# Performance work log

Hardware: AMD Instinct MI355X
Metric: run time of the kernel (lower is better)

The kernel has to match this reference:

```python
import jax, jax.numpy as jnp
import numpy as np
from jax import lax

B, T, D = 2, 2048, 2048
H = 8
DK = D // H          # head_qk_dim = 256 (expand_k forced to 1.0)
DV = D // H          # head_v_dim = 256 (expand_v forced to 1.0)
CONV_K = 4
CHUNK = 64
EPS = 1e-5
INTER = 2816         # int(2048*2*2/3)=2730 -> round up to multiple of 256


def setup_inputs() -> dict:
    key = jax.random.key(0)
    ks = jax.random.split(key, 14)
    s = 0.02
    return {
        "hidden_states": jax.random.normal(ks[0], (B, T, D), jnp.float32),
        "attn_norm_w": jnp.ones((D,), jnp.float32),
        "Wq": jax.random.normal(ks[1], (D, D), jnp.float32) * s,
        "Wk": jax.random.normal(ks[2], (D, D), jnp.float32) * s,
        "Wv": jax.random.normal(ks[3], (D, D), jnp.float32) * s,
        "Wg": jax.random.normal(ks[4], (D, D), jnp.float32) * s,
        "Wo": jax.random.normal(ks[5], (D, D), jnp.float32) * s,
        "conv_wq": jax.random.normal(ks[6], (D, CONV_K), jnp.float32) * 0.3,
        "conv_wk": jax.random.normal(ks[7], (D, CONV_K), jnp.float32) * 0.3,
        "conv_wv": jax.random.normal(ks[8], (D, CONV_K), jnp.float32) * 0.3,
        "gnorm_w": jnp.ones((DV,), jnp.float32),
        "mlp_norm_w": jnp.ones((D,), jnp.float32),
        "W_gate": jax.random.normal(ks[9], (D, 2 * INTER), jnp.float32) * s,
        "W_down": jax.random.normal(ks[10], (INTER, D), jnp.float32) * s,
    }


def rmsnorm(x, w, eps=EPS):
    return x * lax.rsqrt(jnp.mean(x * x, axis=-1, keepdims=True) + eps) * w


def short_conv_silu(x, w):
    # depthwise causal conv1d, kernel CONV_K, no bias, then SiLU. x: [B,T,C], w: [C,K]
    K = w.shape[-1]
    xp = jnp.pad(x, ((0, 0), (K - 1, 0), (0, 0)))
    y = sum(xp[:, i:i + x.shape[1], :] * w[None, None, :, i] for i in range(K))
    return jax.nn.silu(y)


def rope(x, cos, sin):
    # non-interleaved (GPT-NeoX style) rotary over full head dim. x: [B,T,H,d]
    x1, x2 = jnp.split(x, 2, axis=-1)
    c = cos[None, :, None, :]
    s = sin[None, :, None, :]
    return jnp.concatenate([x1 * c - x2 * s, x2 * c + x1 * s], axis=-1)


def chunk_retention(q, k, v, gamma, C=CHUNK):
    # q,k,v: [B,T,H,d]; gamma: [H]. o_t = q_t @ S_t, S_t = gamma*S_{t-1} + k_t^T v_t
    b, t, h, dk = q.shape
    dv = v.shape[-1]
    q = q * (dk ** -0.5)
    n = t // C
    to_chunks = lambda x: x.reshape(b, n, C, h, -1).transpose(1, 0, 3, 2, 4)  # [n,B,H,C,d]
    qc, kc, vc = map(to_chunks, (q, k, v))
    i = jnp.arange(C)
    diff = i[:, None] - i[None, :]
    pe = jnp.where(diff >= 0, diff, 0).astype(q.dtype)
    Dm = jnp.where(diff >= 0, gamma[:, None, None] ** pe, 0.0)       # [H,C,C] intra-chunk decay
    di = gamma[:, None] ** (i + 1).astype(q.dtype)                    # [H,C] decay from prev state
    dkc = gamma[:, None] ** (C - 1 - i).astype(q.dtype)               # [H,C] decay to chunk end
    gC = gamma ** C                                                   # [H]

    def step(S, xs):
        qi, ki, vi = xs                                              # [B,H,C,d]
        A = jnp.einsum('bhid,bhjd->bhij', qi, ki) * Dm
        o = A @ vi + jnp.einsum('bhid,bhde->bhie', qi, S) * di[None, :, :, None]
        S = S * gC[None, :, None, None] + jnp.einsum('bhjd,bhje->bhde', ki * dkc[None, :, :, None], vi)
        return S, o

    S0 = jnp.zeros((b, h, dk, dv), q.dtype)
    _, oc = lax.scan(step, S0, (qc, kc, vc))                          # [n,B,H,C,dv]
    return oc.transpose(1, 0, 3, 2, 4).reshape(b, t, h, dv)


def reference(hidden_states, attn_norm_w, Wq, Wk, Wv, Wg, Wo,
              conv_wq, conv_wk, conv_wv, gnorm_w, mlp_norm_w, W_gate, W_down):
    b, t, d = hidden_states.shape
    # --- MultiScaleRetention block (pre-norm) ---
    x = rmsnorm(hidden_states, attn_norm_w)
    q = short_conv_silu(x @ Wq, conv_wq)
    k = short_conv_silu(x @ Wk, conv_wk)
    v = short_conv_silu(x @ Wv, conv_wv)
    q = q.reshape(b, t, H, DK)
    k = k.reshape(b, t, H, DK)
    v = v.reshape(b, t, H, DV)
    # rotary embedding (base 10000), seqlen_offset=0
    inv_freq = 1.0 / (10000.0 ** (jnp.arange(0, DK, 2, dtype=jnp.float32) / DK))
    freqs = jnp.arange(t, dtype=jnp.float32)[:, None] * inv_freq[None, :]   # [T,DK/2]
    cos, sin = jnp.cos(freqs), jnp.sin(freqs)
    q, k = rope(q, cos, sin), rope(k, cos, sin)
    # per-head retention decay: gamma_h = 1 - 2^(-5-h)
    gamma = 1.0 - jnp.exp2(-5.0 - jnp.arange(H, dtype=jnp.float32))
    o = chunk_retention(q, k, v, gamma)                                     # [B,T,H,DV]
    # fused RMSNorm + swish gate
    g = (x @ Wg).reshape(b, t, H, DV)
    o = rmsnorm(o, gnorm_w) * (g * jax.nn.sigmoid(g))
    o = o.reshape(b, t, d) @ Wo
    h = hidden_states + o
    # --- gated MLP block (pre-norm, SwiGLU) ---
    y = rmsnorm(h, mlp_norm_w)
    gy = y @ W_gate
    gate, yv = jnp.split(gy, 2, axis=-1)
    y = (gate * jax.nn.sigmoid(gate) * yv) @ W_down
    return h + y
```

## Files before the change

### kernel.cpp

```cpp
#include <hip/hip_runtime.h>
#include <hip/hip_bf16.h>
#include <cstdint>
#include <cstddef>
#include <type_traits>


typedef __hip_bfloat16 bf16;
typedef __bf16 bf16x8 __attribute__((ext_vector_type(8)));
typedef __bf16 bf16x4 __attribute__((ext_vector_type(4)));
typedef float f32x4 __attribute__((ext_vector_type(4)));

#define DEVI __device__ __forceinline__

DEVI float bf2f(bf16 x) { return __bfloat162float(x); }
DEVI bf16 f2bf(float x) { return __float2bfloat16(x); }
DEVI float siluf(float x) { return x / (1.f + __expf(-x)); }
DEVI float log2gamma(int h) {
  return log1pf(-exp2f(-5.f - (float)h)) * 1.4426950408889634f;
}

#define GLL16(gp, lp)                                                  \
  __builtin_amdgcn_global_load_lds(                                    \
      (__attribute__((address_space(1))) void*)(gp),                   \
      (__attribute__((address_space(3))) void*)(lp), 16, 0, 0)

DEVI float blockSum256(float v) {
  #pragma unroll
  for (int off = 32; off; off >>= 1) v += __shfl_down(v, off, 64);
  __shared__ float sm[4];
  int lane = threadIdx.x & 63, w = threadIdx.x >> 6;
  if (lane == 0) sm[w] = v;
  __syncthreads();
  return sm[0] + sm[1] + sm[2] + sm[3];
}

__global__ void rmsnorm_k(const float* __restrict__ x, const float* __restrict__ w,
                          bf16* __restrict__ out) {
  long row = blockIdx.x;
  const float* xr = x + row * 2048;
  int i0 = threadIdx.x * 4;
  float4 v0 = *(const float4*)(xr + i0);
  float4 v1 = *(const float4*)(xr + 1024 + i0);
  float ss = v0.x*v0.x + v0.y*v0.y + v0.z*v0.z + v0.w*v0.w
           + v1.x*v1.x + v1.y*v1.y + v1.z*v1.z + v1.w*v1.w;
  ss = blockSum256(ss);
  float s = rsqrtf(ss * (1.f/2048.f) + 1e-5f);
  bf16* orow = out + row * 2048;
  orow[i0+0] = f2bf(v0.x*s*w[i0+0]); orow[i0+1] = f2bf(v0.y*s*w[i0+1]);
  orow[i0+2] = f2bf(v0.z*s*w[i0+2]); orow[i0+3] = f2bf(v0.w*s*w[i0+3]);
  orow[1024+i0+0] = f2bf(v1.x*s*w[1024+i0+0]); orow[1024+i0+1] = f2bf(v1.y*s*w[1024+i0+1]);
  orow[1024+i0+2] = f2bf(v1.z*s*w[1024+i0+2]); orow[1024+i0+3] = f2bf(v1.w*s*w[1024+i0+3]);
}

__global__ void rope_init(float2* __restrict__ tab) {
  int t = blockIdx.x, j = threadIdx.x;
  double inv = exp((double)(-j) * (9.210340371976184 / 128.0));
  double ang = fmod((double)t * inv, 6.283185307179586);
  tab[t * 128 + j] = make_float2((float)cos(ang), (float)sin(ang));
}

__global__ void transpose_w(const float* __restrict__ in, bf16* __restrict__ out,
                            int R, int C) {
  __shared__ float tile[32][33];
  int bx = blockIdx.x * 32, by = blockIdx.y * 32;
  int tx = threadIdx.x, ty = threadIdx.y;
  #pragma unroll
  for (int i = 0; i < 32; i += 8)
    tile[ty + i][tx] = in[(long)(by + ty + i) * C + bx + tx];
  __syncthreads();
  #pragma unroll
  for (int i = 0; i < 32; i += 8)
    out[(long)(bx + ty + i) * R + by + tx] = f2bf(tile[tx][ty + i]);
}

__global__ void transpose_w4(const float* __restrict__ w0, const float* __restrict__ w1,
                             const float* __restrict__ w2, const float* __restrict__ w3,
                             bf16* __restrict__ out) {
  __shared__ float tile[32][33];
  const float* in = blockIdx.z == 0 ? w0 : blockIdx.z == 1 ? w1
                   : blockIdx.z == 2 ? w2 : w3;
  int bx = blockIdx.x * 32, by = blockIdx.y * 32;
  int tx = threadIdx.x, ty = threadIdx.y;
  #pragma unroll
  for (int i = 0; i < 32; i += 8)
    tile[ty + i][tx] = in[(long)(by + ty + i) * 2048 + bx + tx];
  __syncthreads();
  long rbase = (long)blockIdx.z * 2048;
  #pragma unroll
  for (int i = 0; i < 32; i += 8)
    out[(rbase + bx + ty + i) * 2048 + by + tx] = f2bf(tile[tx][ty + i]);
}

__global__ void transpose_head(const bf16* __restrict__ in, bf16* __restrict__ out,
                               int withDecay) {
  __shared__ bf16 tile[32][33];
  const int bh = blockIdx.z, hh = bh & 7;
  const float lg = log2gamma(hh);
  const int t0 = blockIdx.y * 32, d0 = blockIdx.x * 32;
  const int tx = threadIdx.x, ty = threadIdx.y;
  const bf16* src = in + (long)bh * 2048 * 256;
  bf16* dst = out + (long)bh * 2048 * 256;
  #pragma unroll
  for (int i = 0; i < 32; i += 8) {
    int t = t0 + ty + i;
    float v = bf2f(src[(long)t * 256 + d0 + tx]);
    if (withDecay) v *= exp2f(lg * (float)(63 - (t & 63)));
    tile[ty + i][tx] = f2bf(v);
  }
  __syncthreads();
  #pragma unroll
  for (int i = 0; i < 32; i += 8)
    dst[(long)(d0 + ty + i) * 2048 + t0 + tx] = tile[tx][ty + i];
}

template <typename OUT_T, bool DO_ADD>
__global__ __launch_bounds__(256) void gemm_bt(
    const bf16* __restrict__ A, const bf16* __restrict__ Bt,
    OUT_T* __restrict__ C, int ldc, bf16* __restrict__ C2, int split,
    const float* __restrict__ addend, int M, int N, int K) {
  __shared__ alignas(16) bf16 As[128 * 32];
  __shared__ alignas(16) bf16 Bs[128 * 32];
  const int tid = threadIdx.x;
  const int lane = tid & 63, wid = tid >> 6;
  const int quad = lane >> 4, l16 = lane & 15;
  const int wm = wid >> 1, wn = wid & 1;
  const long bm = (long)blockIdx.x * 128;
  const long bn = (long)blockIdx.y * 128;

  const int srow = wid * 16 + (lane >> 2);
  const int scolP = (lane & 3) * 8;
  const int scolG = (((lane & 3) ^ ((srow >> 1) & 3))) * 8;
  const bf16* pa0 = A + (bm + srow) * (long)K + scolG;
  const bf16* pa1 = A + (bm + 64 + srow) * (long)K + scolG;
  const bf16* pb0 = Bt + (bn + srow) * (long)K + scolG;
  const bf16* pb1 = Bt + (bn + 64 + srow) * (long)K + scolG;
  bf16* la0 = As + srow * 32 + scolP;
  bf16* la1 = As + (64 + srow) * 32 + scolP;
  bf16* lb0 = Bs + srow * 32 + scolP;
  bf16* lb1 = Bs + (64 + srow) * 32 + scolP;

  const int fcol = ((quad ^ ((l16 >> 1) & 3)) * 8);

  const f32x4 zz = {0.f, 0.f, 0.f, 0.f};
  f32x4 acc[4][4];
  #pragma unroll
  for (int i = 0; i < 4; i++)
    #pragma unroll
    for (int j = 0; j < 4; j++) acc[i][j] = zz;

  for (int k0 = 0; k0 < K; k0 += 32) {
    GLL16(pa0 + k0, la0);
    GLL16(pa1 + k0, la1);
    GLL16(pb0 + k0, lb0);
    GLL16(pb1 + k0, lb1);
    __syncthreads();
    bf16x8 a[4], b[4];
    #pragma unroll
    for (int i = 0; i < 4; i++)
      a[i] = *(const bf16x8*)(As + (wm * 64 + i * 16 + l16) * 32 + fcol);
    #pragma unroll
    for (int j = 0; j < 4; j++)
      b[j] = *(const bf16x8*)(Bs + (wn * 64 + j * 16 + l16) * 32 + fcol);
    #pragma unroll
    for (int i = 0; i < 4; i++)
      #pragma unroll
      for (int j = 0; j < 4; j++)
        acc[i][j] = __builtin_amdgcn_mfma_f32_16x16x32_bf16(a[i], b[j], acc[i][j], 0, 0, 0);
    __syncthreads();
  }

  const bool sec = (bn >= split);
  #pragma unroll
  for (int i = 0; i < 4; i++)
    #pragma unroll
    for (int j = 0; j < 4; j++)
      #pragma unroll
      for (int r = 0; r < 4; r++) {
        long row = bm + wm * 64 + i * 16 + quad * 4 + r;
        long col = bn + wn * 64 + j * 16 + l16;
        float v = acc[i][j][r];
        if (sec) {
          C2[row * 2048 + (col - split)] = f2bf(v);
        } else {
          if constexpr (DO_ADD) v += addend[row * (long)ldc + col];
          if constexpr (std::is_same<OUT_T, float>::value)
            C[row * (long)ldc + col] = v;
          else
            C[row * (long)ldc + col] = f2bf(v);
        }
      }
}

__global__ void conv3(const bf16* __restrict__ u3,
                      const float* __restrict__ cwq, const float* __restrict__ cwk,
                      const float* __restrict__ cwv, const float2* __restrict__ rtab,
                      bf16* __restrict__ qb, bf16* __restrict__ kb,
                      bf16* __restrict__ vb) {
  const int bt = blockIdx.x;
  const int t = bt & 2047;
  const int b = bt >> 11;
  const int z = blockIdx.y;
  const int tid = threadIdx.x;
  const int h = tid >> 5;
  if (z < 2) {
    const float* cw = z == 0 ? cwq : cwk;
    bf16* out = z == 0 ? qb : kb;
    const float scale = z == 0 ? 0.0625f : 1.0f;
    const int j0 = (tid & 31) * 4;
    const int ch1 = h * 256 + j0, ch2 = ch1 + 128;
    const int c1 = z * 2048 + ch1, c2 = c1 + 128;
    f32x4 w1[4], w2[4];
    #pragma unroll
    for (int e = 0; e < 4; e++) {
      w1[e] = *(const f32x4*)(cw + (ch1 + e) * 4);
      w2[e] = *(const f32x4*)(cw + (ch2 + e) * 4);
    }
    float a1[4] = {0.f, 0.f, 0.f, 0.f}, a2[4] = {0.f, 0.f, 0.f, 0.f};
    #pragma unroll
    for (int i = 0; i < 4; i++) {
      int ts = t - 3 + i;
      if (ts >= 0) {
        const bf16* up = u3 + (long)(bt - 3 + i) * 6144;
        bf16x4 v1 = *(const bf16x4*)(up + c1);
        bf16x4 v2 = *(const bf16x4*)(up + c2);
        #pragma unroll
        for (int e = 0; e < 4; e++) {
          a1[e] += (float)v1[e] * w1[e][i];
          a2[e] += (float)v2[e] * w2[e][i];
        }
      }
    }
    f32x4 r01 = *(const f32x4*)(rtab + t * 128 + j0);
    f32x4 r23 = *(const f32x4*)(rtab + t * 128 + j0 + 2);
    float cs[4] = {r01[0], r01[2], r23[0], r23[2]};
    float sn[4] = {r01[1], r01[3], r23[1], r23[3]};
    bf16x4 o1, o2;
    #pragma unroll
    for (int e = 0; e < 4; e++) {
      float s1 = siluf(a1[e]), s2 = siluf(a2[e]);
      o1[e] = (__bf16)((s1 * cs[e] - s2 * sn[e]) * scale);
      o2[e] = (__bf16)((s2 * cs[e] + s1 * sn[e]) * scale);
    }
    long obase = ((long)(b * 8 + h) * 2048 + t) * 256;
    *(bf16x4*)(out + obase + j0) = o1;
    *(bf16x4*)(out + obase + 128 + j0) = o2;
  } else {
    const int e0 = (tid & 31) * 8;
    const int ch = h * 256 + e0;
    const int c = 4096 + ch;
    f32x4 w[8];
    #pragma unroll
    for (int e = 0; e < 8; e++) w[e] = *(const f32x4*)(cwv + (ch + e) * 4);
    float a[8] = {0.f, 0.f, 0.f, 0.f, 0.f, 0.f, 0.f, 0.f};
    #pragma unroll
    for (int i = 0; i < 4; i++) {
      int ts = t - 3 + i;
      if (ts >= 0) {
        bf16x8 v = *(const bf16x8*)(u3 + (long)(bt - 3 + i) * 6144 + c);
        #pragma unroll
        for (int e = 0; e < 8; e++) a[e] += (float)v[e] * w[e][i];
      }
    }
    bf16x8 o;
    #pragma unroll
    for (int e = 0; e < 8; e++) o[e] = (__bf16)siluf(a[e]);
    *(bf16x8*)(vb + ((long)(b * 8 + h) * 2048 + t) * 256 + e0) = o;
  }
}

__global__ __launch_bounds__(256) void chunk_outer(
    const bf16* __restrict__ vT, const bf16* __restrict__ kTd,
    bf16* __restrict__ states) {
  __shared__ alignas(16) bf16 lk[256 * 72];
  const int chunk = blockIdx.x, bh = blockIdx.y;
  const int tid = threadIdx.x;
  const int lane = tid & 63, wid = tid >> 6;
  const int quad = lane >> 4, l16 = lane & 15;
  const long base = (long)bh * 256 * 2048 + chunk * 64;

  #pragma unroll
  for (int it = 0; it < 8; it++) {
    int r = it * 32 + (tid >> 3);
    int cb = tid & 7;
    *(int4*)(lk + r * 72 + cb * 8) = *(const int4*)(kTd + base + (long)r * 2048 + cb * 8);
  }
  bf16x8 a[4][2];
  #pragma unroll
  for (int i = 0; i < 4; i++)
    #pragma unroll
    for (int ks = 0; ks < 2; ks++)
      a[i][ks] = *(const bf16x8*)(vT + base + (long)(wid * 64 + i * 16 + l16) * 2048 +
                                  ks * 32 + quad * 8);
  __syncthreads();

  bf16* sout = states + ((long)bh * 32 + chunk) * 65536;
  const f32x4 zz = {0.f, 0.f, 0.f, 0.f};
  for (int g = 0; g < 4; g++) {
    f32x4 acc[4][4];
    #pragma unroll
    for (int i = 0; i < 4; i++)
      #pragma unroll
      for (int j = 0; j < 4; j++) acc[i][j] = zz;
    #pragma unroll
    for (int ks = 0; ks < 2; ks++) {
      bf16x8 b[4];
      #pragma unroll
      for (int j = 0; j < 4; j++)
        b[j] = *(const bf16x8*)(lk + (g * 64 + j * 16 + l16) * 72 + ks * 32 + quad * 8);
      #pragma unroll
      for (int i = 0; i < 4; i++)
        #pragma unroll
        for (int j = 0; j < 4; j++)
          acc[i][j] = __builtin_amdgcn_mfma_f32_16x16x32_bf16(a[i][ks], b[j], acc[i][j], 0, 0, 0);
    }
    #pragma unroll
    for (int i = 0; i < 4; i++)
      #pragma unroll
      for (int j = 0; j < 4; j++)
        #pragma unroll
        for (int r = 0; r < 4; r++) {
          int e = wid * 64 + i * 16 + quad * 4 + r;
          int d = g * 64 + j * 16 + l16;
          sout[(long)e * 256 + d] = f2bf(acc[i][j][r]);
        }
  }
}

__global__ void state_scan(bf16* __restrict__ states) {
  const int bh = blockIdx.y, h = bh & 7;
  const float gC = exp2f(64.f * log2gamma(h));
  long idx = ((long)blockIdx.x * 256 + threadIdx.x) * 8;
  bf16* p = states + (long)bh * 32 * 65536 + idx;
  float s[8] = {0.f, 0.f, 0.f, 0.f, 0.f, 0.f, 0.f, 0.f};
  for (int n = 0; n < 32; n++) {
    bf16x8 m = *(const bf16x8*)(p + (long)n * 65536);
    bf16x8 o;
    #pragma unroll
    for (int e = 0; e < 8; e++) {
      o[e] = (__bf16)s[e];
      s[e] = gC * s[e] + (float)m[e];
    }
    *(bf16x8*)(p + (long)n * 65536) = o;
  }
}

__global__ __launch_bounds__(256) void chunk_inner(
    const bf16* __restrict__ q, const bf16* __restrict__ k,
    const bf16* __restrict__ vT, const bf16* __restrict__ ST,
    const bf16* __restrict__ g, const float* __restrict__ gw,
    bf16* __restrict__ og) {
  __shared__ alignas(16) bf16 P[64 * 328];
  __shared__ float sq[64][4];
  __shared__ float sscale[64];
  const int chunk = blockIdx.x, bh = blockIdx.y;
  const int b_ = bh >> 3, h = bh & 7;
  const float lg = log2gamma(h);
  const int tid = threadIdx.x;
  const int lane = tid & 63, wid = tid >> 6;
  const int quad = lane >> 4, l16 = lane & 15;
  const long qkbase = ((long)bh * 2048 + chunk * 64) * 256;

  {
    const int row = tid >> 2, cb = tid & 3;
    const float di = exp2f(lg * (float)(row + 1));
    const bf16* qs = q + qkbase + (long)row * 256 + cb * 64;
    bf16* pd = P + row * 328 + 64 + cb * 64;
    #pragma unroll
    for (int mb = 0; mb < 8; mb++) {
      bf16x8 v = *(const bf16x8*)(qs + mb * 8);
      #pragma unroll
      for (int e = 0; e < 8; e++) pd[mb * 8 + e] = f2bf((float)v[e] * di);
    }
  }

  {
    const f32x4 zz = {0.f, 0.f, 0.f, 0.f};
    f32x4 acc[4];
    #pragma unroll
    for (int j = 0; j < 4; j++) acc[j] = zz;
    #pragma unroll
    for (int ks = 0; ks < 8; ks++) {
      bf16x8 a = *(const bf16x8*)(q + qkbase + (long)(wid * 16 + l16) * 256 + ks * 32 + quad * 8);
      #pragma unroll
      for (int j = 0; j < 4; j++) {
        bf16x8 b = *(const bf16x8*)(k + qkbase + (long)(j * 16 + l16) * 256 + ks * 32 + quad * 8);
        acc[j] = __builtin_amdgcn_mfma_f32_16x16x32_bf16(a, b, acc[j], 0, 0, 0);
      }
    }
    #pragma unroll
    for (int j = 0; j < 4; j++)
      #pragma unroll
      for (int r = 0; r < 4; r++) {
        int il = wid * 16 + quad * 4 + r;
        int jl = j * 16 + l16;
        int dd = il - jl;
        float v = (dd >= 0) ? acc[j][r] * exp2f(lg * (float)dd) : 0.f;
        P[il * 328 + jl] = f2bf(v);
      }
  }
  __syncthreads();

  const f32x4 zz = {0.f, 0.f, 0.f, 0.f};
  f32x4 acc[4][4];
  #pragma unroll
  for (int i = 0; i < 4; i++)
    #pragma unroll
    for (int j = 0; j < 4; j++) acc[i][j] = zz;
  const long vbase = (long)bh * 256 * 2048 + chunk * 64;
  const long sbase = ((long)bh * 32 + chunk) * 65536;
  #pragma unroll
  for (int ks = 0; ks < 10; ks++) {
    bf16x8 a[4];
    #pragma unroll
    for (int i = 0; i < 4; i++)
      a[i] = *(const bf16x8*)(P + (i * 16 + l16) * 328 + ks * 32 + quad * 8);
    int kk = ks * 32 + quad * 8;
    bf16x8 b[4];
    #pragma unroll
    for (int j = 0; j < 4; j++) {
      int e = wid * 64 + j * 16 + l16;
      const bf16* src = (kk < 64) ? (vT + vbase + (long)e * 2048 + kk)
                                  : (ST + sbase + (long)e * 256 + (kk - 64));
      b[j] = *(const bf16x8*)src;
    }
    #pragma unroll
    for (int i = 0; i < 4; i++)
      #pragma unroll
      for (int j = 0; j < 4; j++)
        acc[i][j] = __builtin_amdgcn_mfma_f32_16x16x32_bf16(a[i], b[j], acc[i][j], 0, 0, 0);
  }

  #pragma unroll
  for (int i = 0; i < 4; i++)
    #pragma unroll
    for (int r = 0; r < 4; r++) {
      float s = acc[i][0][r]*acc[i][0][r] + acc[i][1][r]*acc[i][1][r]
              + acc[i][2][r]*acc[i][2][r] + acc[i][3][r]*acc[i][3][r];
      s += __shfl_xor(s, 1, 64);
      s += __shfl_xor(s, 2, 64);
      s += __shfl_xor(s, 4, 64);
      s += __shfl_xor(s, 8, 64);
      if (l16 == 0) sq[i * 16 + quad * 4 + r][wid] = s;
    }
  __syncthreads();
  if (tid < 64) {
    float t = sq[tid][0] + sq[tid][1] + sq[tid][2] + sq[tid][3];
    sscale[tid] = rsqrtf(t * (1.f/256.f) + 1e-5f);
  }
  __syncthreads();

  #pragma unroll
  for (int i = 0; i < 4; i++)
    #pragma unroll
    for (int j = 0; j < 4; j++) {
      int e = wid * 64 + j * 16 + l16;
      float w = gw[e];
      #pragma unroll
      for (int r = 0; r < 4; r++) {
        int row = i * 16 + quad * 4 + r;
        long bt = (long)b_ * 2048 + chunk * 64 + row;
        float gg = bf2f(g[bt * 2048 + h * 256 + e]);
        float val = acc[i][j][r] * sscale[row] * w * siluf(gg);
        og[bt * 2048 + h * 256 + e] = f2bf(val);
      }
    }
}

__global__ void swiglu_k(const bf16* __restrict__ gy, bf16* __restrict__ act) {
  long i = (long)blockIdx.x * 256 + threadIdx.x;
  long m = i / 2816, c = i - m * 2816;
  float gv = bf2f(gy[m * 5632 + c]);
  float vv = bf2f(gy[m * 5632 + 2816 + c]);
  act[i] = f2bf(siluf(gv) * vv);
}

extern "C" void kernel_launch(void* const* d_in, const int* in_sizes, int n_in,
                              void* d_out, int out_size, void* d_ws, size_t ws_size,
                              hipStream_t stream) {
  (void)in_sizes; (void)n_in; (void)out_size;
  const float* hidden = (const float*)d_in[0];
  const float* attn_w = (const float*)d_in[1];
  const float* Wq = (const float*)d_in[2];
  const float* Wk = (const float*)d_in[3];
  const float* Wv = (const float*)d_in[4];
  const float* Wg = (const float*)d_in[5];
  const float* Wo = (const float*)d_in[6];
  const float* cwq = (const float*)d_in[7];
  const float* cwk = (const float*)d_in[8];
  const float* cwv = (const float*)d_in[9];
  const float* gnw = (const float*)d_in[10];
  const float* mlpw = (const float*)d_in[11];
  const float* Wgate = (const float*)d_in[12];
  const float* Wdown = (const float*)d_in[13];
  float* out = (float*)d_out;
  char* ws = (char*)d_ws;

  if (ws_size < 209715200ull) return;

  const size_t MB16 = 16777216ull;
  char* WTr = ws;
  bf16* WT4    = (bf16*)WTr;
  bf16* kTb    = (bf16*)WTr;
  bf16* WoT    = (bf16*)WTr;
  bf16* WgateT = (bf16*)WTr;
  bf16* WdownT = (bf16*)WTr;
  bf16* og     = (bf16*)(WTr + MB16);
  char* Ur = ws + 33554432ull;
  bf16*  u3     = (bf16*)Ur;
  bf16*  xbf    = (bf16*)(Ur + 50331648ull);
  bf16*  states = (bf16*)Ur;
  float* hbuf   = (float*)Ur;
  bf16*  act    = (bf16*)(Ur + 33554432ull);
  char* Qr = ws + 100663296ull;
  bf16* qb  = (bf16*)Qr;
  bf16* kb  = (bf16*)(Qr + MB16);
  bf16* vTb = (bf16*)(Qr + 2 * MB16);
  bf16* vnb = (bf16*)(Qr + 3 * MB16);
  bf16* gy  = (bf16*)Qr;
  bf16* ybf = (bf16*)(Qr + 50331648ull);
  bf16* g   = (bf16*)(ws + 167772160ull);
  float2* rtab = (float2*)(ws + 184549376ull);

  dim3 tb32(32, 8);

  rope_init<<<2048, 128, 0, stream>>>(rtab);
  rmsnorm_k<<<4096, 256, 0, stream>>>(hidden, attn_w, xbf);

  transpose_w4<<<dim3(64, 64, 4), tb32, 0, stream>>>(Wq, Wk, Wv, Wg, WT4);
  gemm_bt<bf16, false><<<dim3(32, 64), 256, 0, stream>>>(
      xbf, WT4, u3, 6144, g, 6144, nullptr, 4096, 8192, 2048);

  conv3<<<dim3(4096, 3), 256, 0, stream>>>(u3, cwq, cwk, cwv, rtab, qb, kb, vnb);
  transpose_head<<<dim3(8, 64, 16), tb32, 0, stream>>>(kb, kTb, 1);
  transpose_head<<<dim3(8, 64, 16), tb32, 0, stream>>>(vnb, vTb, 0);

  chunk_outer<<<dim3(32, 16), 256, 0, stream>>>(vTb, kTb, states);
  state_scan<<<dim3(32, 16), 256, 0, stream>>>(states);
  chunk_inner<<<dim3(32, 16), 256, 0, stream>>>(qb, kb, vTb, states, g, gnw, og);

  transpose_w<<<dim3(64, 64), tb32, 0, stream>>>(Wo, WoT, 2048, 2048);
  gemm_bt<float, true><<<dim3(32, 16), 256, 0, stream>>>(
      og, WoT, hbuf, 2048, nullptr, 1 << 30, hidden, 4096, 2048, 2048);

  rmsnorm_k<<<4096, 256, 0, stream>>>(hbuf, mlpw, ybf);
  transpose_w<<<dim3(176, 64), tb32, 0, stream>>>(Wgate, WgateT, 2048, 5632);
  gemm_bt<bf16, false><<<dim3(32, 44), 256, 0, stream>>>(
      ybf, WgateT, gy, 5632, nullptr, 1 << 30, nullptr, 4096, 5632, 2048);
  swiglu_k<<<45056, 256, 0, stream>>>(gy, act);
  transpose_w<<<dim3(64, 88), tb32, 0, stream>>>(Wdown, WdownT, 2816, 2048);
  gemm_bt<float, true><<<dim3(32, 16), 256, 0, stream>>>(
      act, WdownT, out, 2048, nullptr, 1 << 30, hbuf, 4096, 2048, 2816);
}
```

Baseline: 859.1 us.

## Fuse SwiGLU into gate GEMM epilogue and deepen GEMM K-tile to 64

Rewrites the gate/up weight transpose so gate and value columns interleave in 16-column groups. The gate GEMM epilogue can then pair adjacent accumulator tiles and write silu(gate)*val directly, which removes the separate swiglu kernel and the round trip of the 4096x5632 intermediate. It also doubles the GEMM K step to 64 with a new XOR swizzle, halving barrier count per K. The larger LDS tiles may reduce occupancy, and the K step must divide K (2816 = 44*64 holds).

```diff
diff --git a/kernel.cpp b/kernel.cpp
--- a/kernel.cpp
+++ b/kernel.cpp
@@ -91,6 +91,22 @@
     out[(rbase + bx + ty + i) * 2048 + by + tx] = f2bf(tile[tx][ty + i]);
 }
 
+__global__ void transpose_wgate(const float* __restrict__ in, bf16* __restrict__ out) {
+  __shared__ float tile[32][33];
+  int bx = blockIdx.x * 32, by = blockIdx.y * 32;
+  int tx = threadIdx.x, ty = threadIdx.y;
+  int r = bx + tx;
+  int gidx = r >> 4;
+  int scol = ((gidx & 1) ? 2816 : 0) + ((gidx >> 1) << 4) + (r & 15);
+  #pragma unroll
+  for (int i = 0; i < 32; i += 8)
+    tile[ty + i][tx] = in[(long)(by + ty + i) * 5632 + scol];
+  __syncthreads();
+  #pragma unroll
+  for (int i = 0; i < 32; i += 8)
+    out[(long)(bx + ty + i) * 2048 + by + tx] = f2bf(tile[tx][ty + i]);
+}
+
 __global__ void transpose_head(const bf16* __restrict__ in, bf16* __restrict__ out,
                                int withDecay) {
   __shared__ bf16 tile[32][33];
@@ -113,13 +129,13 @@
     dst[(long)(d0 + ty + i) * 2048 + t0 + tx] = tile[tx][ty + i];
 }
 
-template <typename OUT_T, bool DO_ADD>
+template <typename OUT_T, bool DO_ADD, bool DO_SWIGLU>
 __global__ __launch_bounds__(256) void gemm_bt(
     const bf16* __restrict__ A, const bf16* __restrict__ Bt,
     OUT_T* __restrict__ C, int ldc, bf16* __restrict__ C2, int split,
     const float* __restrict__ addend, int M, int N, int K) {
-  __shared__ alignas(16) bf16 As[128 * 32];
-  __shared__ alignas(16) bf16 Bs[128 * 32];
+  __shared__ alignas(16) bf16 As[128 * 64];
+  __shared__ alignas(16) bf16 Bs[128 * 64];
   const int tid = threadIdx.x;
   const int lane = tid & 63, wid = tid >> 6;
   const int quad = lane >> 4, l16 = lane & 15;
@@ -127,19 +143,18 @@
   const long bm = (long)blockIdx.x * 128;
   const long bn = (long)blockIdx.y * 128;
 
-  const int srow = wid * 16 + (lane >> 2);
-  const int scolP = (lane & 3) * 8;
-  const int scolG = (((lane & 3) ^ ((srow >> 1) & 3))) * 8;
-  const bf16* pa0 = A + (bm + srow) * (long)K + scolG;
-  const bf16* pa1 = A + (bm + 64 + srow) * (long)K + scolG;
-  const bf16* pb0 = Bt + (bn + srow) * (long)K + scolG;
-  const bf16* pb1 = Bt + (bn + 64 + srow) * (long)K + scolG;
-  bf16* la0 = As + srow * 32 + scolP;
-  bf16* la1 = As + (64 + srow) * 32 + scolP;
-  bf16* lb0 = Bs + srow * 32 + scolP;
-  bf16* lb1 = Bs + (64 + srow) * 32 + scolP;
-
-  const int fcol = ((quad ^ ((l16 >> 1) & 3)) * 8);
+  const int srow = wid * 8 + (lane >> 3);
+  const int scb = lane & 7;
+  const int scbG = scb ^ (lane >> 3);
+  const bf16* pa[4]; const bf16* pb[4]; bf16* la[4]; bf16* lb[4];
+  #pragma unroll
+  for (int c = 0; c < 4; c++) {
+    int row = c * 32 + srow;
+    pa[c] = A + (bm + row) * (long)K + scbG * 8;
+    pb[c] = Bt + (bn + row) * (long)K + scbG * 8;
+    la[c] = As + row * 64 + scb * 8;
+    lb[c] = Bs + row * 64 + scb * 8;
+  }
 
   const f32x4 zz = {0.f, 0.f, 0.f, 0.f};
   f32x4 acc[4][4];
@@ -148,47 +163,69 @@
     #pragma unroll
     for (int j = 0; j < 4; j++) acc[i][j] = zz;
 
-  for (int k0 = 0; k0 < K; k0 += 32) {
-    GLL16(pa0 + k0, la0);
-    GLL16(pa1 + k0, la1);
-    GLL16(pb0 + k0, lb0);
-    GLL16(pb1 + k0, lb1);
+  const int l7 = l16 & 7;
+  for (int k0 = 0; k0 < K; k0 += 64) {
+    #pragma unroll
+    for (int c = 0; c < 4; c++) {
+      GLL16(pa[c] + k0, la[c]);
+      GLL16(pb[c] + k0, lb[c]);
+    }
     __syncthreads();
-    bf16x8 a[4], b[4];
+    #pragma unroll
+    for (int ks = 0; ks < 2; ks++) {
+      const int fcol = ((ks * 4 + quad) ^ l7) * 8;
+      bf16x8 a[4], b[4];
+      #pragma unroll
+      for (int i = 0; i < 4; i++)
+        a[i] = *(const bf16x8*)(As + (wm * 64 + i * 16 + l16) * 64 + fcol);
+      #pragma unroll
+      for (int j = 0; j < 4; j++)
+        b[j] = *(const bf16x8*)(Bs + (wn * 64 + j * 16 + l16) * 64 + fcol);
+      #pragma unroll
+      for (int i = 0; i < 4; i++)
+        #pragma unroll
+        for (int j = 0; j < 4; j++)
+          acc[i][j] = __builtin_amdgcn_mfma_f32_16x16x32_bf16(a[i], b[j], acc[i][j], 0, 0, 0);
+    }
+    __syncthreads();
+  }
+
+  if constexpr (DO_SWIGLU) {
     #pragma unroll
     for (int i = 0; i < 4; i++)
-      a[i] = *(const bf16x8*)(As + (wm * 64 + i * 16 + l16) * 32 + fcol);
-    #pragma unroll
-    for (int j = 0; j < 4; j++)
-      b[j] = *(const bf16x8*)(Bs + (wn * 64 + j * 16 + l16) * 32 + fcol);
-    #pragma unroll
-    for (int i = 0; i < 4; i++)
-      #pragma unroll
-      for (int j = 0; j < 4; j++)
-        acc[i][j] = __builtin_amdgcn_mfma_f32_16x16x32_bf16(a[i], b[j], acc[i][j], 0, 0, 0);
-    __syncthreads();
-  }
-
-  const bool sec = (bn >= split);
-  #pragma unroll
-  for (int i = 0; i < 4; i++)
-    #pragma unroll
-    for (int j = 0; j < 4; j++)
-      #pragma unroll
-      for (int r = 0; r < 4; r++) {
-        long row = bm + wm * 64 + i * 16 + quad * 4 + r;
-        long col = bn + wn * 64 + j * 16 + l16;
-        float v = acc[i][j][r];
-        if (sec) {
-          C2[row * 2048 + (col - split)] = f2bf(v);
-        } else {
-          if constexpr (DO_ADD) v += addend[row * (long)ldc + col];
-          if constexpr (std::is_same<OUT_T, float>::value)
-            C[row * (long)ldc + col] = v;
-          else
-            C[row * (long)ldc + col] = f2bf(v);
+      #pragma unroll
+      for (int jp = 0; jp < 2; jp++) {
+        long acol = bn / 2 + wn * 32 + jp * 16 + l16;
+        #pragma unroll
+        for (int r = 0; r < 4; r++) {
+          long row = bm + wm * 64 + i * 16 + quad * 4 + r;
+          float gate = acc[i][2 * jp][r];
+          float val = acc[i][2 * jp + 1][r];
+          C2[row * 2816 + acol] = f2bf(siluf(gate) * val);
         }
       }
+  } else {
+    const bool sec = (bn >= split);
+    #pragma unroll
+    for (int i = 0; i < 4; i++)
+      #pragma unroll
+      for (int j = 0; j < 4; j++)
+        #pragma unroll
+        for (int r = 0; r < 4; r++) {
+          long row = bm + wm * 64 + i * 16 + quad * 4 + r;
+          long col = bn + wn * 64 + j * 16 + l16;
+          float v = acc[i][j][r];
+          if (sec) {
+            C2[row * 2048 + (col - split)] = f2bf(v);
+          } else {
+            if constexpr (DO_ADD) v += addend[row * (long)ldc + col];
+            if constexpr (std::is_same<OUT_T, float>::value)
+              C[row * (long)ldc + col] = v;
+            else
+              C[row * (long)ldc + col] = f2bf(v);
+          }
+        }
+  }
 }
 
 __global__ void conv3(const bf16* __restrict__ u3,
@@ -464,14 +501,6 @@
         og[bt * 2048 + h * 256 + e] = f2bf(val);
       }
     }
-}
-
-__global__ void swiglu_k(const bf16* __restrict__ gy, bf16* __restrict__ act) {
-  long i = (long)blockIdx.x * 256 + threadIdx.x;
-  long m = i / 2816, c = i - m * 2816;
-  float gv = bf2f(gy[m * 5632 + c]);
-  float vv = bf2f(gy[m * 5632 + 2816 + c]);
-  act[i] = f2bf(siluf(gv) * vv);
 }
 
 extern "C" void kernel_launch(void* const* d_in, const int* in_sizes, int n_in,
@@ -516,7 +545,6 @@
   bf16* kb  = (bf16*)(Qr + MB16);
   bf16* vTb = (bf16*)(Qr + 2 * MB16);
   bf16* vnb = (bf16*)(Qr + 3 * MB16);
-  bf16* gy  = (bf16*)Qr;
   bf16* ybf = (bf16*)(Qr + 50331648ull);
   bf16* g   = (bf16*)(ws + 167772160ull);
   float2* rtab = (float2*)(ws + 184549376ull);
@@ -527,7 +555,7 @@
   rmsnorm_k<<<4096, 256, 0, stream>>>(hidden, attn_w, xbf);
 
   transpose_w4<<<dim3(64, 64, 4), tb32, 0, stream>>>(Wq, Wk, Wv, Wg, WT4);
-  gemm_bt<bf16, false><<<dim3(32, 64), 256, 0, stream>>>(
+  gemm_bt<bf16, false, false><<<dim3(32, 64), 256, 0, stream>>>(
       xbf, WT4, u3, 6144, g, 6144, nullptr, 4096, 8192, 2048);
 
   conv3<<<dim3(4096, 3), 256, 0, stream>>>(u3, cwq, cwk, cwv, rtab, qb, kb, vnb);
@@ -539,15 +567,14 @@
   chunk_inner<<<dim3(32, 16), 256, 0, stream>>>(qb, kb, vTb, states, g, gnw, og);
 
   transpose_w<<<dim3(64, 64), tb32, 0, stream>>>(Wo, WoT, 2048, 2048);
-  gemm_bt<float, true><<<dim3(32, 16), 256, 0, stream>>>(
+  gemm_bt<float, true, false><<<dim3(32, 16), 256, 0, stream>>>(
       og, WoT, hbuf, 2048, nullptr, 1 << 30, hidden, 4096, 2048, 2048);
 
   rmsnorm_k<<<4096, 256, 0, stream>>>(hbuf, mlpw, ybf);
-  transpose_w<<<dim3(176, 64), tb32, 0, stream>>>(Wgate, WgateT, 2048, 5632);
-  gemm_bt<bf16, false><<<dim3(32, 44), 256, 0, stream>>>(
-      ybf, WgateT, gy, 5632, nullptr, 1 << 30, nullptr, 4096, 5632, 2048);
-  swiglu_k<<<45056, 256, 0, stream>>>(gy, act);
+  transpose_wgate<<<dim3(176, 64), tb32, 0, stream>>>(Wgate, WgateT);
+  gemm_bt<bf16, false, true><<<dim3(32, 44), 256, 0, stream>>>(
+      ybf, WgateT, nullptr, 2816, act, 1 << 30, nullptr, 4096, 5632, 2048);
   transpose_w<<<dim3(64, 88), tb32, 0, stream>>>(Wdown, WdownT, 2816, 2048);
-  gemm_bt<float, true><<<dim3(32, 16), 256, 0, stream>>>(
+  gemm_bt<float, true, false><<<dim3(32, 16), 256, 0, stream>>>(
       act, WdownT, out, 2048, nullptr, 1 << 30, hbuf, 4096, 2048, 2816);
 }
```

Result: faster. 795.1 us (-7.4%).
